# Kernel optimization log

Measured on AMD Instinct MI355X. Metric: run time of the kernel, lower is better.

Reference implementation:

```python
import jax, jax.numpy as jnp
import numpy as np
from jax import lax

DK, K = 3, 3          # duration_kernel_size, kernel_size
PD, P = 1, 1          # duration_padding, padding
RANKS = 3


def setup_inputs() -> dict:
    key = jax.random.key(0)
    k1, k2, k3, k4, k5 = jax.random.split(key, 5)
    B, Cin, Cout, D, H, W = 2, 64, 64, 8, 128, 128
    x = jax.random.normal(k1, (B, Cin, D, H, W), dtype=jnp.float32)
    # 1x1x1 conv weights (squeezed to [out, in])
    head_w = jax.random.normal(k2, (Cout, Cin), dtype=jnp.float32) * 0.1
    tail_w = jax.random.normal(k3, (Cout, Cout), dtype=jnp.float32) * 0.1
    std = float(np.sqrt(2.0 / RANKS))
    U_w = jax.random.normal(k4, (DK * K * K, RANKS), dtype=jnp.float32) * std
    V_w = jax.random.normal(k5, (Cout, RANKS), dtype=jnp.float32) * std
    return {"x": x, "head_w": head_w, "tail_w": tail_w, "U_w": U_w, "V_w": V_w}


def _forward(x, head_w, tail_w, U_w, V_w):
    B, Cin, D, H, W = x.shape
    Cout = head_w.shape[0]
    R = U_w.shape[1]
    # head 1x1x1 conv
    h = jnp.einsum('bidhw,oi->bodhw', x, head_w)
    # replicate pad (torch F.pad mode='replicate' == jnp.pad mode='edge')
    hp = jnp.pad(h, ((0, 0), (0, 0), (PD, PD), (P, P), (P, P)), mode='edge')
    # einsum('bcdhwk,kr->bcdhwr') over unfolded windows == depthwise conv with
    # a kernel shared across channels: fold (B,C) into the batch dim and run a
    # 1->R channel 3D correlation (avoids materializing the [.,27] unfold tensor).
    xin = hp.reshape(B * Cout, 1, D + 2 * PD, H + 2 * P, W + 2 * P)
    kern = U_w.T.reshape(R, 1, DK, K, K)  # unfold flattens as (dk, kh, kw)
    Up = lax.conv_general_dilated(
        xin, kern, window_strides=(1, 1, 1), padding='VALID',
        dimension_numbers=('NCDHW', 'OIDHW', 'NCDHW'))
    Up = Up.reshape(B, Cout, R, D, H, W)
    # _l2norm over rank dim: u / (1e-6 + ||u||_2)
    norm = jnp.sqrt(jnp.sum(Up * Up, axis=2, keepdims=True))
    Un = Up / (1e-6 + norm)
    # V projection: einsum('bcdhwk,cr->brdhwk') with k==1
    Vp = jnp.einsum('bcdhw,cr->brdhw', h, V_w)
    # UV: einsum('bcdhwr,brdhwk->bcdhwk') with k==1 -> contract over r
    UV = jnp.einsum('bcrdhw,brdhw->bcdhw', Un, Vp)
    # tail 1x1x1 conv
    out = jnp.einsum('bcdhw,oc->bodhw', UV, tail_w)
    return out


def reference(x, head_w, tail_w, U_w, V_w):
    return _forward(x, head_w, tail_w, U_w, V_w)
```

## Files before the change

### kernel.cpp

```cpp
#include <hip/hip_runtime.h>

#define Bn   2
#define Cn   64
#define Dd   8
#define Hd   128
#define Wd   128
#define HW   16384
#define DHW  131072
#define NPOS 262144
#define NELEM 16777216

typedef __attribute__((ext_vector_type(8))) short short8;
typedef __attribute__((ext_vector_type(4))) float floatx4;

__device__ __forceinline__ short f2bf(float f) {
    union { float f; unsigned u; } v; v.f = f;
    unsigned r = (v.u + 0x7FFFu + ((v.u >> 16) & 1u)) >> 16;
    return (short)r;
}
__device__ __forceinline__ float bf2f(short s) {
    union { unsigned u; float f; } v; v.u = ((unsigned)(unsigned short)s) << 16;
    return v.f;
}
__device__ __forceinline__ void split2(float f, short& hi, short& lo) {
    union { float f; unsigned u; } a; a.f = f;
    unsigned hu = a.u & 0xFFFF0000u;
    hi = (short)(hu >> 16);
    union { unsigned u; float f; } hb; hb.u = hu;
    union { float f; unsigned u; } lb; lb.f = f - hb.f;
    lo = (short)(lb.u >> 16);
}

__global__ __launch_bounds__(256) void k_prep(const float* __restrict__ head_w,
                                              const float* __restrict__ tail_w,
                                              const float* __restrict__ V_w,
                                              short* __restrict__ Whh, short* __restrict__ Whl,
                                              short* __restrict__ Wth, short* __restrict__ Wtl)
{
    int t = threadIdx.x;
#pragma unroll
    for (int rep = 0; rep < 16; ++rep) {
        int idx = rep * 256 + t;
        short hh, hl;
        split2(head_w[idx], hh, hl);
        Whh[idx] = hh; Whl[idx] = hl;
        split2(tail_w[idx], hh, hl);
        Wth[idx] = hh; Wtl[idx] = hl;
    }
    if (t < 192) {
        int r = t >> 6, i = t & 63;
        float s = 0.f;
        for (int cc = 0; cc < 64; ++cc) s += V_w[cc * 3 + r] * head_w[cc * 64 + i];
        short hh, hl;
        split2(s, hh, hl);
        Whh[(64 + r) * 64 + i] = hh;
        Whl[(64 + r) * 64 + i] = hl;
    }
#pragma unroll
    for (int rep = 0; rep < 4; ++rep) {
        int idx = rep * 256 + t;
        if (idx < 832) { Whh[67 * 64 + idx] = 0; Whl[67 * 64 + idx] = 0; }
    }
}

__global__ __launch_bounds__(256) void k_headm(const float* __restrict__ x,
                                               const short* __restrict__ Whh,
                                               const short* __restrict__ Whl,
                                               float* __restrict__ h,
                                               float* __restrict__ Vp)
{
    __shared__ __align__(16) char smem[52 * 1024];
    short* Xh = (short*)smem;
    short* Xl = (short*)(smem + 16 * 1024);
    short* Bh = (short*)(smem + 32 * 1024);
    short* Bl = (short*)(smem + 42 * 1024);
    float* Cb = (float*)smem;

    int t  = threadIdx.x;
    int p0 = blockIdx.x * 128;
    int b  = p0 >> 17;
    int s0 = p0 & (DHW - 1);
    const float* xb = x + ((size_t)b * Cn) * DHW + s0;

    int pp = t & 127;
    int ho = t >> 7;
#pragma unroll
    for (int pass = 0; pass < 4; ++pass) {
        int in0 = pass * 16 + ho * 8;
        short8 vh, vl;
#pragma unroll
        for (int j = 0; j < 8; ++j) {
            short hh, hl;
            split2(xb[(size_t)(in0 + j) * DHW + pp], hh, hl);
            vh[j] = hh; vl[j] = hl;
        }
        int blk  = ((in0 >> 5) << 3) | (pp >> 4);
        int slot = (((in0 >> 3) & 3) << 4) | (pp & 15);
        *(short8*)&Xh[(blk * 64 + slot) * 8] = vh;
        *(short8*)&Xl[(blk * 64 + slot) * 8] = vl;
    }
#pragma unroll
    for (int pass = 0; pass < 3; ++pass) {
        int unit = pass * 256 + t;
        if (unit < 640) {
            int o   = unit - (unit / 80) * 80;
            int oc  = unit / 80;
            int in0 = oc * 8;
            int blk  = ((o >> 4) << 1) | (in0 >> 5);
            int slot = (((in0 >> 3) & 3) << 4) | (o & 15);
            *(short8*)&Bh[(blk * 64 + slot) * 8] = *(const short8*)&Whh[o * 64 + in0];
            *(short8*)&Bl[(blk * 64 + slot) * 8] = *(const short8*)&Whl[o * 64 + in0];
        }
    }
    __syncthreads();

    int lane = t & 63;
    int w    = t >> 6;
    floatx4 acc[2][5];
#pragma unroll
    for (int mt = 0; mt < 2; ++mt)
#pragma unroll
        for (int nt = 0; nt < 5; ++nt) acc[mt][nt] = (floatx4)0.f;

    const short8* XhV = (const short8*)Xh;
    const short8* XlV = (const short8*)Xl;
    const short8* BhV = (const short8*)Bh;
    const short8* BlV = (const short8*)Bl;
#pragma unroll
    for (int ks = 0; ks < 2; ++ks) {
        short8 ah0 = XhV[(ks * 8 + w * 2 + 0) * 64 + lane];
        short8 ah1 = XhV[(ks * 8 + w * 2 + 1) * 64 + lane];
        short8 al0 = XlV[(ks * 8 + w * 2 + 0) * 64 + lane];
        short8 al1 = XlV[(ks * 8 + w * 2 + 1) * 64 + lane];
#pragma unroll
        for (int nt = 0; nt < 5; ++nt) {
            short8 bh = BhV[(nt * 2 + ks) * 64 + lane];
            short8 bl = BlV[(nt * 2 + ks) * 64 + lane];
            acc[0][nt] = __builtin_amdgcn_mfma_f32_16x16x32_bf16(al0, bh, acc[0][nt], 0, 0, 0);
            acc[0][nt] = __builtin_amdgcn_mfma_f32_16x16x32_bf16(ah0, bl, acc[0][nt], 0, 0, 0);
            acc[0][nt] = __builtin_amdgcn_mfma_f32_16x16x32_bf16(ah0, bh, acc[0][nt], 0, 0, 0);
            acc[1][nt] = __builtin_amdgcn_mfma_f32_16x16x32_bf16(al1, bh, acc[1][nt], 0, 0, 0);
            acc[1][nt] = __builtin_amdgcn_mfma_f32_16x16x32_bf16(ah1, bl, acc[1][nt], 0, 0, 0);
            acc[1][nt] = __builtin_amdgcn_mfma_f32_16x16x32_bf16(ah1, bh, acc[1][nt], 0, 0, 0);
        }
    }

    __syncthreads();
    int outc = lane & 15;
    int quad = lane >> 4;
#pragma unroll
    for (int mt = 0; mt < 2; ++mt)
#pragma unroll
        for (int nt = 0; nt < 5; ++nt) {
            int o   = nt * 16 + outc;
            int pos = w * 32 + mt * 16 + quad * 4;
            *(floatx4*)&Cb[o * 132 + pos] = acc[mt][nt];
        }
    __syncthreads();

    int xr = (t & 31) * 4;
    int ob = t >> 5;
#pragma unroll
    for (int pass = 0; pass < 9; ++pass) {
        int o = pass * 8 + ob;
        floatx4 vv = *(const floatx4*)&Cb[o * 132 + xr];
        if (o < 64) {
            *(floatx4*)&h[((size_t)(b * Cn + o)) * DHW + s0 + xr] = vv;
        } else if (o < 67) {
            *(floatx4*)&Vp[((size_t)(b * 3 + (o - 64))) * DHW + s0 + xr] = vv;
        }
    }
}

__global__ __launch_bounds__(256) void k_uv(const float* __restrict__ h,
                                            const float* __restrict__ Vp,
                                            const float* __restrict__ U_w,
                                            unsigned short* __restrict__ UVq)
{
    __shared__ float tile[Dd][4][Wd];

    int blk = blockIdx.x;
    int yt  = blk & 63;
    int bc  = blk >> 6;
    int b   = bc >> 6;
    int y0  = yt * 2;
    int t   = threadIdx.x;

    const float* hb = h + (size_t)bc * DHW;
#pragma unroll
    for (int rep = 0; rep < 4; ++rep) {
        int idx = rep * 256 + t;
        int d   = idx >> 7;
        int rem = idx & 127;
        int yr  = rem >> 5;
        int x4  = (rem & 31) * 4;
        int zy  = y0 - 1 + yr;
        zy = zy < 0 ? 0 : (zy > Hd - 1 ? Hd - 1 : zy);
        *(floatx4*)&tile[d][yr][x4] = *(const floatx4*)(hb + d * HW + zy * Wd + x4);
    }
    __syncthreads();

    int xx = t & 127;
    int yr = t >> 7;
    int y  = y0 + yr;
    int xm = xx - 1; if (xm < 0) xm = 0;
    int xp = xx + 1; if (xp > Wd - 1) xp = Wd - 1;

    float a0[8], a1[8], a2[8];
#pragma unroll
    for (int d = 0; d < 8; ++d) { a0[d] = 0.f; a1[d] = 0.f; a2[d] = 0.f; }

#define CONTRIB(dd, dk)                                                   \
    {                                                                     \
        _Pragma("unroll")                                                 \
        for (int kh = 0; kh < 3; ++kh) {                                  \
            _Pragma("unroll")                                             \
            for (int kw = 0; kw < 3; ++kw) {                              \
                const int kk = (((dk) * 3 + kh) * 3 + kw) * 3;            \
                a0[dd] += v[kh][kw] * U_w[kk + 0];                        \
                a1[dd] += v[kh][kw] * U_w[kk + 1];                        \
                a2[dd] += v[kh][kw] * U_w[kk + 2];                        \
            }                                                             \
        }                                                                 \
    }

#pragma unroll
    for (int sl = 0; sl < 8; ++sl) {
        float v[3][3];
#pragma unroll
        for (int kh = 0; kh < 3; ++kh) {
            const float* row = &tile[sl][yr + kh][0];
            v[kh][0] = row[xm]; v[kh][1] = row[xx]; v[kh][2] = row[xp];
        }
        CONTRIB(sl, 1);
        if (sl == 0) CONTRIB(0, 0);
        if (sl < 7)  CONTRIB(sl + 1, 0);
        if (sl > 0)  CONTRIB(sl - 1, 2);
        if (sl == 7) CONTRIB(7, 2);
    }
#undef CONTRIB

    const float* vpb    = Vp + (size_t)b * 3 * DHW + y * Wd + xx;
    unsigned short* uvb = UVq + (size_t)bc * DHW + y * Wd + xx;
#pragma unroll
    for (int d = 0; d < 8; ++d) {
        float nrm = sqrtf(a0[d] * a0[d] + a1[d] * a1[d] + a2[d] * a2[d]);
        float inv = 1.f / (1e-6f + nrm);
        float uv = (a0[d] * vpb[(size_t)d * HW]
                  + a1[d] * vpb[(size_t)DHW + d * HW]
                  + a2[d] * vpb[(size_t)2 * DHW + d * HW]) * inv;
        uvb[(size_t)d * HW] = (unsigned short)f2bf(uv);
    }
}

__global__ __launch_bounds__(256) void k_tailm(const unsigned short* __restrict__ UVq,
                                               const short* __restrict__ Wth,
                                               const short* __restrict__ Wtl,
                                               float* __restrict__ out)
{
    __shared__ __align__(16) char smem[34 * 1024];
    short* Xh = (short*)smem;
    short* Bh = (short*)(smem + 16 * 1024);
    short* Bl = (short*)(smem + 24 * 1024);
    float* Cb = (float*)smem;

    int t  = threadIdx.x;
    int p0 = blockIdx.x * 128;
    int b  = p0 >> 17;
    int s0 = p0 & (DHW - 1);
    const unsigned short* uq = UVq + ((size_t)b * Cn) * DHW + s0;

    int pp = t & 127;
    int ho = t >> 7;
#pragma unroll
    for (int pass = 0; pass < 4; ++pass) {
        int in0 = pass * 16 + ho * 8;
        short8 vh;
#pragma unroll
        for (int j = 0; j < 8; ++j)
            vh[j] = (short)uq[(size_t)(in0 + j) * DHW + pp];
        int blk  = ((in0 >> 5) << 3) | (pp >> 4);
        int slot = (((in0 >> 3) & 3) << 4) | (pp & 15);
        *(short8*)&Xh[(blk * 64 + slot) * 8] = vh;
    }
#pragma unroll
    for (int pass = 0; pass < 2; ++pass) {
        int unit = pass * 256 + t;
        int o    = unit & 63;
        int oc   = unit >> 6;
        int in0  = oc * 8;
        int blk  = ((o >> 4) << 1) | (in0 >> 5);
        int slot = (((in0 >> 3) & 3) << 4) | (o & 15);
        *(short8*)&Bh[(blk * 64 + slot) * 8] = *(const short8*)&Wth[o * 64 + in0];
        *(short8*)&Bl[(blk * 64 + slot) * 8] = *(const short8*)&Wtl[o * 64 + in0];
    }
    __syncthreads();

    int lane = t & 63;
    int w    = t >> 6;
    floatx4 acc[2][4];
#pragma unroll
    for (int mt = 0; mt < 2; ++mt)
#pragma unroll
        for (int nt = 0; nt < 4; ++nt) acc[mt][nt] = (floatx4)0.f;

    const short8* XhV = (const short8*)Xh;
    const short8* BhV = (const short8*)Bh;
    const short8* BlV = (const short8*)Bl;
#pragma unroll
    for (int ks = 0; ks < 2; ++ks) {
        short8 ah0 = XhV[(ks * 8 + w * 2 + 0) * 64 + lane];
        short8 ah1 = XhV[(ks * 8 + w * 2 + 1) * 64 + lane];
#pragma unroll
        for (int nt = 0; nt < 4; ++nt) {
            short8 bh = BhV[(nt * 2 + ks) * 64 + lane];
            short8 bl = BlV[(nt * 2 + ks) * 64 + lane];
            acc[0][nt] = __builtin_amdgcn_mfma_f32_16x16x32_bf16(ah0, bl, acc[0][nt], 0, 0, 0);
            acc[0][nt] = __builtin_amdgcn_mfma_f32_16x16x32_bf16(ah0, bh, acc[0][nt], 0, 0, 0);
            acc[1][nt] = __builtin_amdgcn_mfma_f32_16x16x32_bf16(ah1, bl, acc[1][nt], 0, 0, 0);
            acc[1][nt] = __builtin_amdgcn_mfma_f32_16x16x32_bf16(ah1, bh, acc[1][nt], 0, 0, 0);
        }
    }

    __syncthreads();
    int outc = lane & 15;
    int quad = lane >> 4;
#pragma unroll
    for (int mt = 0; mt < 2; ++mt)
#pragma unroll
        for (int nt = 0; nt < 4; ++nt) {
            int o   = nt * 16 + outc;
            int pos = w * 32 + mt * 16 + quad * 4;
            *(floatx4*)&Cb[o * 132 + pos] = acc[mt][nt];
        }
    __syncthreads();

    int xr = (t & 31) * 4;
    int ob = t >> 5;
#pragma unroll
    for (int pass = 0; pass < 8; ++pass) {
        int o = pass * 8 + ob;
        floatx4 vv = *(const floatx4*)&Cb[o * 132 + xr];
        *(floatx4*)&out[((size_t)(b * Cn + o)) * DHW + s0 + xr] = vv;
    }
}

extern "C" void kernel_launch(void* const* d_in, const int* in_sizes, int n_in,
                              void* d_out, int out_size, void* d_ws, size_t ws_size,
                              hipStream_t stream)
{
    const float* x      = (const float*)d_in[0];
    const float* head_w = (const float*)d_in[1];
    const float* tail_w = (const float*)d_in[2];
    const float* U_w    = (const float*)d_in[3];
    const float* V_w    = (const float*)d_in[4];
    float* out = (float*)d_out;

    float* h   = (float*)d_ws;
    float* Vp  = h + (size_t)NELEM;
    unsigned short* UVq = (unsigned short*)(Vp + (size_t)Bn * 3 * DHW);
    short* Whh = (short*)(UVq + (size_t)NELEM);
    short* Whl = Whh + 80 * 64;
    short* Wth = Whl + 80 * 64;
    short* Wtl = Wth + 64 * 64;

    k_prep<<<1, 256, 0, stream>>>(head_w, tail_w, V_w, Whh, Whl, Wth, Wtl);
    k_headm<<<NPOS / 128, 256, 0, stream>>>(x, Whh, Whl, h, Vp);
    k_uv<<<Bn * Cn * (Hd / 2), 256, 0, stream>>>(h, Vp, U_w, UVq);
    k_tailm<<<NPOS / 128, 256, 0, stream>>>(UVq, Wth, Wtl, out);
}
```

Before: 220.1 us.

## Load MFMA A-operands directly from global and store accumulators without LDS staging

In the head and tail 1x1 conv kernels, each lane now reads its MFMA A-fragment straight from global memory into registers instead of staging a transposed tile through shared memory. Each lane also writes its accumulator fragments directly to global instead of going through an LDS transpose buffer. This removes LDS traffic, two barriers and the shared-memory footprint, which may raise occupancy. The cost is less coalesced access: reads become 16-lane strided gathers and writes become 16-byte chunks spread across channel rows.

Result: slower. 230.9 us (+4.9%).

```diff
diff --git a/kernel.cpp b/kernel.cpp
--- a/kernel.cpp
+++ b/kernel.cpp
@@ -12,6 +12,7 @@
 
 typedef __attribute__((ext_vector_type(8))) short short8;
 typedef __attribute__((ext_vector_type(4))) float floatx4;
+typedef __attribute__((ext_vector_type(4))) unsigned short ushort4v;
 
 __device__ __forceinline__ short f2bf(float f) {
     union { float f; unsigned u; } v; v.f = f;
@@ -69,36 +70,32 @@
                                                float* __restrict__ h,
                                                float* __restrict__ Vp)
 {
-    __shared__ __align__(16) char smem[52 * 1024];
-    short* Xh = (short*)smem;
-    short* Xl = (short*)(smem + 16 * 1024);
-    short* Bh = (short*)(smem + 32 * 1024);
-    short* Bl = (short*)(smem + 42 * 1024);
-    float* Cb = (float*)smem;
-
-    int t  = threadIdx.x;
+    __shared__ __align__(16) short Bh[80 * 64];
+    __shared__ __align__(16) short Bl[80 * 64];
+
+    int t    = threadIdx.x;
+    int lane = t & 63;
+    int w    = t >> 6;
     int p0 = blockIdx.x * 128;
     int b  = p0 >> 17;
     int s0 = p0 & (DHW - 1);
     const float* xb = x + ((size_t)b * Cn) * DHW + s0;
 
-    int pp = t & 127;
-    int ho = t >> 7;
-#pragma unroll
-    for (int pass = 0; pass < 4; ++pass) {
-        int in0 = pass * 16 + ho * 8;
-        short8 vh, vl;
-#pragma unroll
-        for (int j = 0; j < 8; ++j) {
-            short hh, hl;
-            split2(xb[(size_t)(in0 + j) * DHW + pp], hh, hl);
-            vh[j] = hh; vl[j] = hl;
-        }
-        int blk  = ((in0 >> 5) << 3) | (pp >> 4);
-        int slot = (((in0 >> 3) & 3) << 4) | (pp & 15);
-        *(short8*)&Xh[(blk * 64 + slot) * 8] = vh;
-        *(short8*)&Xl[(blk * 64 + slot) * 8] = vl;
-    }
+    int ch0 = (lane >> 4) * 8;
+    int px  = w * 32 + (lane & 15);
+
+    short8 ah[2][2], al[2][2];
+#pragma unroll
+    for (int ks = 0; ks < 2; ++ks)
+#pragma unroll
+        for (int mt = 0; mt < 2; ++mt)
+#pragma unroll
+            for (int j = 0; j < 8; ++j) {
+                short hh, hl;
+                split2(xb[(size_t)(ks * 32 + ch0 + j) * DHW + px + mt * 16], hh, hl);
+                ah[ks][mt][j] = hh; al[ks][mt][j] = hl;
+            }
+
 #pragma unroll
     for (int pass = 0; pass < 3; ++pass) {
         int unit = pass * 256 + t;
@@ -114,38 +111,28 @@
     }
     __syncthreads();
 
-    int lane = t & 63;
-    int w    = t >> 6;
     floatx4 acc[2][5];
 #pragma unroll
     for (int mt = 0; mt < 2; ++mt)
 #pragma unroll
         for (int nt = 0; nt < 5; ++nt) acc[mt][nt] = (floatx4)0.f;
 
-    const short8* XhV = (const short8*)Xh;
-    const short8* XlV = (const short8*)Xl;
     const short8* BhV = (const short8*)Bh;
     const short8* BlV = (const short8*)Bl;
 #pragma unroll
-    for (int ks = 0; ks < 2; ++ks) {
-        short8 ah0 = XhV[(ks * 8 + w * 2 + 0) * 64 + lane];
-        short8 ah1 = XhV[(ks * 8 + w * 2 + 1) * 64 + lane];
-        short8 al0 = XlV[(ks * 8 + w * 2 + 0) * 64 + lane];
-        short8 al1 = XlV[(ks * 8 + w * 2 + 1) * 64 + lane];
+    for (int ks = 0; ks < 2; ++ks)
 #pragma unroll
         for (int nt = 0; nt < 5; ++nt) {
             short8 bh = BhV[(nt * 2 + ks) * 64 + lane];
             short8 bl = BlV[(nt * 2 + ks) * 64 + lane];
-            acc[0][nt] = __builtin_amdgcn_mfma_f32_16x16x32_bf16(al0, bh, acc[0][nt], 0, 0, 0);
-            acc[0][nt] = __builtin_amdgcn_mfma_f32_16x16x32_bf16(ah0, bl, acc[0][nt], 0, 0, 0);
-            acc[0][nt] = __builtin_amdgcn_mfma_f32_16x16x32_bf16(ah0, bh, acc[0][nt], 0, 0, 0);
-            acc[1][nt] = __builtin_amdgcn_mfma_f32_16x16x32_bf16(al1, bh, acc[1][nt], 0, 0, 0);
-            acc[1][nt] = __builtin_amdgcn_mfma_f32_16x16x32_bf16(ah1, bl, acc[1][nt], 0, 0, 0);
-            acc[1][nt] = __builtin_amdgcn_mfma_f32_16x16x32_bf16(ah1, bh, acc[1][nt], 0, 0, 0);
-        }
-    }
-
-    __syncthreads();
+            acc[0][nt] = __builtin_amdgcn_mfma_f32_16x16x32_bf16(al[ks][0], bh, acc[0][nt], 0, 0, 0);
+            acc[0][nt] = __builtin_amdgcn_mfma_f32_16x16x32_bf16(ah[ks][0], bl, acc[0][nt], 0, 0, 0);
+            acc[0][nt] = __builtin_amdgcn_mfma_f32_16x16x32_bf16(ah[ks][0], bh, acc[0][nt], 0, 0, 0);
+            acc[1][nt] = __builtin_amdgcn_mfma_f32_16x16x32_bf16(al[ks][1], bh, acc[1][nt], 0, 0, 0);
+            acc[1][nt] = __builtin_amdgcn_mfma_f32_16x16x32_bf16(ah[ks][1], bl, acc[1][nt], 0, 0, 0);
+            acc[1][nt] = __builtin_amdgcn_mfma_f32_16x16x32_bf16(ah[ks][1], bh, acc[1][nt], 0, 0, 0);
+        }
+
     int outc = lane & 15;
     int quad = lane >> 4;
 #pragma unroll
@@ -153,23 +140,13 @@
 #pragma unroll
         for (int nt = 0; nt < 5; ++nt) {
             int o   = nt * 16 + outc;
-            int pos = w * 32 + mt * 16 + quad * 4;
-            *(floatx4*)&Cb[o * 132 + pos] = acc[mt][nt];
-        }
-    __syncthreads();
-
-    int xr = (t & 31) * 4;
-    int ob = t >> 5;
-#pragma unroll
-    for (int pass = 0; pass < 9; ++pass) {
-        int o = pass * 8 + ob;
-        floatx4 vv = *(const floatx4*)&Cb[o * 132 + xr];
-        if (o < 64) {
-            *(floatx4*)&h[((size_t)(b * Cn + o)) * DHW + s0 + xr] = vv;
-        } else if (o < 67) {
-            *(floatx4*)&Vp[((size_t)(b * 3 + (o - 64))) * DHW + s0 + xr] = vv;
-        }
-    }
+            int pos = s0 + w * 32 + mt * 16 + quad * 4;
+            if (o < 64) {
+                *(floatx4*)&h[((size_t)(b * Cn + o)) * DHW + pos] = acc[mt][nt];
+            } else if (o < 67) {
+                *(floatx4*)&Vp[((size_t)(b * 3 + (o - 64))) * DHW + pos] = acc[mt][nt];
+            }
+        }
 }
 
 __global__ __launch_bounds__(256) void k_uv(const float* __restrict__ h,
@@ -258,31 +235,29 @@
                                                const short* __restrict__ Wtl,
                                                float* __restrict__ out)
 {
-    __shared__ __align__(16) char smem[34 * 1024];
-    short* Xh = (short*)smem;
-    short* Bh = (short*)(smem + 16 * 1024);
-    short* Bl = (short*)(smem + 24 * 1024);
-    float* Cb = (float*)smem;
-
-    int t  = threadIdx.x;
+    __shared__ __align__(16) short Bh[64 * 64];
+    __shared__ __align__(16) short Bl[64 * 64];
+
+    int t    = threadIdx.x;
+    int lane = t & 63;
+    int w    = t >> 6;
     int p0 = blockIdx.x * 128;
     int b  = p0 >> 17;
     int s0 = p0 & (DHW - 1);
     const unsigned short* uq = UVq + ((size_t)b * Cn) * DHW + s0;
 
-    int pp = t & 127;
-    int ho = t >> 7;
-#pragma unroll
-    for (int pass = 0; pass < 4; ++pass) {
-        int in0 = pass * 16 + ho * 8;
-        short8 vh;
-#pragma unroll
-        for (int j = 0; j < 8; ++j)
-            vh[j] = (short)uq[(size_t)(in0 + j) * DHW + pp];
-        int blk  = ((in0 >> 5) << 3) | (pp >> 4);
-        int slot = (((in0 >> 3) & 3) << 4) | (pp & 15);
-        *(short8*)&Xh[(blk * 64 + slot) * 8] = vh;
-    }
+    int ch0 = (lane >> 4) * 8;
+    int px  = w * 32 + (lane & 15);
+
+    short8 a[2][2];
+#pragma unroll
+    for (int ks = 0; ks < 2; ++ks)
+#pragma unroll
+        for (int mt = 0; mt < 2; ++mt)
+#pragma unroll
+            for (int j = 0; j < 8; ++j)
+                a[ks][mt][j] = (short)uq[(size_t)(ks * 32 + ch0 + j) * DHW + px + mt * 16];
+
 #pragma unroll
     for (int pass = 0; pass < 2; ++pass) {
         int unit = pass * 256 + t;
@@ -296,33 +271,26 @@
     }
     __syncthreads();
 
-    int lane = t & 63;
-    int w    = t >> 6;
     floatx4 acc[2][4];
 #pragma unroll
     for (int mt = 0; mt < 2; ++mt)
 #pragma unroll
         for (int nt = 0; nt < 4; ++nt) acc[mt][nt] = (floatx4)0.f;
 
-    const short8* XhV = (const short8*)Xh;
     const short8* BhV = (const short8*)Bh;
     const short8* BlV = (const short8*)Bl;
 #pragma unroll
-    for (int ks = 0; ks < 2; ++ks) {
-        short8 ah0 = XhV[(ks * 8 + w * 2 + 0) * 64 + lane];
-        short8 ah1 = XhV[(ks * 8 + w * 2 + 1) * 64 + lane];
+    for (int ks = 0; ks < 2; ++ks)
 #pragma unroll
         for (int nt = 0; nt < 4; ++nt) {
             short8 bh = BhV[(nt * 2 + ks) * 64 + lane];
             short8 bl = BlV[(nt * 2 + ks) * 64 + lane];
-            acc[0][nt] = __builtin_amdgcn_mfma_f32_16x16x32_bf16(ah0, bl, acc[0][nt], 0, 0, 0);
-            acc[0][nt] = __builtin_amdgcn_mfma_f32_16x16x32_bf16(ah0, bh, acc[0][nt], 0, 0, 0);
-            acc[1][nt] = __builtin_amdgcn_mfma_f32_16x16x32_bf16(ah1, bl, acc[1][nt], 0, 0, 0);
-            acc[1][nt] = __builtin_amdgcn_mfma_f32_16x16x32_bf16(ah1, bh, acc[1][nt], 0, 0, 0);
-        }
-    }
-
-    __syncthreads();
+            acc[0][nt] = __builtin_amdgcn_mfma_f32_16x16x32_bf16(a[ks][0], bl, acc[0][nt], 0, 0, 0);
+            acc[0][nt] = __builtin_amdgcn_mfma_f32_16x16x32_bf16(a[ks][0], bh, acc[0][nt], 0, 0, 0);
+            acc[1][nt] = __builtin_amdgcn_mfma_f32_16x16x32_bf16(a[ks][1], bl, acc[1][nt], 0, 0, 0);
+            acc[1][nt] = __builtin_amdgcn_mfma_f32_16x16x32_bf16(a[ks][1], bh, acc[1][nt], 0, 0, 0);
+        }
+
     int outc = lane & 15;
     int quad = lane >> 4;
 #pragma unroll
@@ -330,19 +298,9 @@
 #pragma unroll
         for (int nt = 0; nt < 4; ++nt) {
             int o   = nt * 16 + outc;
-            int pos = w * 32 + mt * 16 + quad * 4;
-            *(floatx4*)&Cb[o * 132 + pos] = acc[mt][nt];
-        }
-    __syncthreads();
-
-    int xr = (t & 31) * 4;
-    int ob = t >> 5;
-#pragma unroll
-    for (int pass = 0; pass < 8; ++pass) {
-        int o = pass * 8 + ob;
-        floatx4 vv = *(const floatx4*)&Cb[o * 132 + xr];
-        *(floatx4*)&out[((size_t)(b * Cn + o)) * DHW + s0 + xr] = vv;
-    }
+            int pos = s0 + w * 32 + mt * 16 + quad * 4;
+            *(floatx4*)&out[((size_t)(b * Cn + o)) * DHW + pos] = acc[mt][nt];
+        }
 }
 
 extern "C" void kernel_launch(void* const* d_in, const int* in_sizes, int n_in,
```

## Halve head-kernel LDS by staging K in two halves and splitting epilogue

Applied to the files above, without the earlier changes.

The head GEMM kernel now stages only half of the input channels in shared memory at a time. The second half is prefetched into registers and overlapped with the first MFMA pass, and the output write-back is split into two smaller staging rounds. This cuts LDS from 52KB to 36KB per block, so more blocks can be resident per CU. In exchange it adds extra barriers, more register pressure from the 16-float prefetch buffer, and an extra epilogue round.

After: 222.5 us. About the same (+1.1%).

```diff
diff --git a/kernel.cpp b/kernel.cpp
--- a/kernel.cpp
+++ b/kernel.cpp
@@ -12,6 +12,7 @@
 
 typedef __attribute__((ext_vector_type(8))) short short8;
 typedef __attribute__((ext_vector_type(4))) float floatx4;
+typedef __attribute__((ext_vector_type(4))) unsigned short ushort4v;
 
 __device__ __forceinline__ short f2bf(float f) {
     union { float f; unsigned u; } v; v.f = f;
@@ -69,11 +70,11 @@
                                                float* __restrict__ h,
                                                float* __restrict__ Vp)
 {
-    __shared__ __align__(16) char smem[52 * 1024];
+    __shared__ __align__(16) char smem[36 * 1024];
     short* Xh = (short*)smem;
-    short* Xl = (short*)(smem + 16 * 1024);
-    short* Bh = (short*)(smem + 32 * 1024);
-    short* Bl = (short*)(smem + 42 * 1024);
+    short* Xl = (short*)(smem + 8 * 1024);
+    short* Bh = (short*)(smem + 16 * 1024);
+    short* Bl = (short*)(smem + 26 * 1024);
     float* Cb = (float*)smem;
 
     int t  = threadIdx.x;
@@ -84,8 +85,17 @@
 
     int pp = t & 127;
     int ho = t >> 7;
-#pragma unroll
-    for (int pass = 0; pass < 4; ++pass) {
+
+    float xreg[16];
+#pragma unroll
+    for (int pass = 0; pass < 2; ++pass) {
+        int in0 = 32 + pass * 16 + ho * 8;
+#pragma unroll
+        for (int j = 0; j < 8; ++j)
+            xreg[pass * 8 + j] = xb[(size_t)(in0 + j) * DHW + pp];
+    }
+#pragma unroll
+    for (int pass = 0; pass < 2; ++pass) {
         int in0 = pass * 16 + ho * 8;
         short8 vh, vl;
 #pragma unroll
@@ -94,7 +104,7 @@
             split2(xb[(size_t)(in0 + j) * DHW + pp], hh, hl);
             vh[j] = hh; vl[j] = hl;
         }
-        int blk  = ((in0 >> 5) << 3) | (pp >> 4);
+        int blk  = pp >> 4;
         int slot = (((in0 >> 3) & 3) << 4) | (pp & 15);
         *(short8*)&Xh[(blk * 64 + slot) * 8] = vh;
         *(short8*)&Xl[(blk * 64 + slot) * 8] = vl;
@@ -126,16 +136,15 @@
     const short8* XlV = (const short8*)Xl;
     const short8* BhV = (const short8*)Bh;
     const short8* BlV = (const short8*)Bl;
-#pragma unroll
-    for (int ks = 0; ks < 2; ++ks) {
-        short8 ah0 = XhV[(ks * 8 + w * 2 + 0) * 64 + lane];
-        short8 ah1 = XhV[(ks * 8 + w * 2 + 1) * 64 + lane];
-        short8 al0 = XlV[(ks * 8 + w * 2 + 0) * 64 + lane];
-        short8 al1 = XlV[(ks * 8 + w * 2 + 1) * 64 + lane];
+    {
+        short8 ah0 = XhV[(w * 2 + 0) * 64 + lane];
+        short8 ah1 = XhV[(w * 2 + 1) * 64 + lane];
+        short8 al0 = XlV[(w * 2 + 0) * 64 + lane];
+        short8 al1 = XlV[(w * 2 + 1) * 64 + lane];
 #pragma unroll
         for (int nt = 0; nt < 5; ++nt) {
-            short8 bh = BhV[(nt * 2 + ks) * 64 + lane];
-            short8 bl = BlV[(nt * 2 + ks) * 64 + lane];
+            short8 bh = BhV[(nt * 2 + 0) * 64 + lane];
+            short8 bl = BlV[(nt * 2 + 0) * 64 + lane];
             acc[0][nt] = __builtin_amdgcn_mfma_f32_16x16x32_bf16(al0, bh, acc[0][nt], 0, 0, 0);
             acc[0][nt] = __builtin_amdgcn_mfma_f32_16x16x32_bf16(ah0, bl, acc[0][nt], 0, 0, 0);
             acc[0][nt] = __builtin_amdgcn_mfma_f32_16x16x32_bf16(ah0, bh, acc[0][nt], 0, 0, 0);
@@ -144,26 +153,80 @@
             acc[1][nt] = __builtin_amdgcn_mfma_f32_16x16x32_bf16(ah1, bh, acc[1][nt], 0, 0, 0);
         }
     }
-
-    __syncthreads();
+    __syncthreads();
+
+#pragma unroll
+    for (int pass = 0; pass < 2; ++pass) {
+        int in0 = pass * 16 + ho * 8;
+        short8 vh, vl;
+#pragma unroll
+        for (int j = 0; j < 8; ++j) {
+            short hh, hl;
+            split2(xreg[pass * 8 + j], hh, hl);
+            vh[j] = hh; vl[j] = hl;
+        }
+        int blk  = pp >> 4;
+        int slot = (((in0 >> 3) & 3) << 4) | (pp & 15);
+        *(short8*)&Xh[(blk * 64 + slot) * 8] = vh;
+        *(short8*)&Xl[(blk * 64 + slot) * 8] = vl;
+    }
+    __syncthreads();
+
+    {
+        short8 ah0 = XhV[(w * 2 + 0) * 64 + lane];
+        short8 ah1 = XhV[(w * 2 + 1) * 64 + lane];
+        short8 al0 = XlV[(w * 2 + 0) * 64 + lane];
+        short8 al1 = XlV[(w * 2 + 1) * 64 + lane];
+#pragma unroll
+        for (int nt = 0; nt < 5; ++nt) {
+            short8 bh = BhV[(nt * 2 + 1) * 64 + lane];
+            short8 bl = BlV[(nt * 2 + 1) * 64 + lane];
+            acc[0][nt] = __builtin_amdgcn_mfma_f32_16x16x32_bf16(al0, bh, acc[0][nt], 0, 0, 0);
+            acc[0][nt] = __builtin_amdgcn_mfma_f32_16x16x32_bf16(ah0, bl, acc[0][nt], 0, 0, 0);
+            acc[0][nt] = __builtin_amdgcn_mfma_f32_16x16x32_bf16(ah0, bh, acc[0][nt], 0, 0, 0);
+            acc[1][nt] = __builtin_amdgcn_mfma_f32_16x16x32_bf16(al1, bh, acc[1][nt], 0, 0, 0);
+            acc[1][nt] = __builtin_amdgcn_mfma_f32_16x16x32_bf16(ah1, bl, acc[1][nt], 0, 0, 0);
+            acc[1][nt] = __builtin_amdgcn_mfma_f32_16x16x32_bf16(ah1, bh, acc[1][nt], 0, 0, 0);
+        }
+    }
+    __syncthreads();
+
     int outc = lane & 15;
     int quad = lane >> 4;
+    int xr = (t & 31) * 4;
+    int ob = t >> 5;
+
 #pragma unroll
     for (int mt = 0; mt < 2; ++mt)
 #pragma unroll
-        for (int nt = 0; nt < 5; ++nt) {
+        for (int nt = 0; nt < 3; ++nt) {
             int o   = nt * 16 + outc;
             int pos = w * 32 + mt * 16 + quad * 4;
             *(floatx4*)&Cb[o * 132 + pos] = acc[mt][nt];
         }
     __syncthreads();
-
-    int xr = (t & 31) * 4;
-    int ob = t >> 5;
-#pragma unroll
-    for (int pass = 0; pass < 9; ++pass) {
+#pragma unroll
+    for (int pass = 0; pass < 6; ++pass) {
         int o = pass * 8 + ob;
         floatx4 vv = *(const floatx4*)&Cb[o * 132 + xr];
+        *(floatx4*)&h[((size_t)(b * Cn + o)) * DHW + s0 + xr] = vv;
+    }
+    __syncthreads();
+
+#pragma unroll
+    for (int mt = 0; mt < 2; ++mt)
+#pragma unroll
+        for (int nt = 3; nt < 5; ++nt) {
+            int o   = nt * 16 + outc;
+            int pos = w * 32 + mt * 16 + quad * 4;
+            *(floatx4*)&Cb[(o - 48) * 132 + pos] = acc[mt][nt];
+        }
+    __syncthreads();
+#pragma unroll
+    for (int pass = 0; pass < 4; ++pass) {
+        int op = pass * 8 + ob;
+        int o  = op + 48;
+        floatx4 vv = *(const floatx4*)&Cb[op * 132 + xr];
         if (o < 64) {
             *(floatx4*)&h[((size_t)(b * Cn + o)) * DHW + s0 + xr] = vv;
         } else if (o < 67) {
```
